# Optimization experiments

Measured on AMD Instinct MI355X. Metric: run time of the kernel, lower is better.

The kernel has to match this reference:

```python
import jax, jax.numpy as jnp
import numpy as np

B, S, D = 4, 1024, 1024
H = 16
HD = D // H  # 64
LN_EPS = 1e-5


def setup_inputs() -> dict:
    key = jax.random.key(0)
    ks = jax.random.split(key, 12)
    s = 1.0 / np.sqrt(D)
    return {
        "x": jax.random.normal(ks[0], (B, S, D), dtype=jnp.float32),
        "wq": jax.random.normal(ks[1], (D, D), dtype=jnp.float32) * s,
        "bq": jnp.zeros((D,), dtype=jnp.float32),
        "wk": jax.random.normal(ks[2], (D, D), dtype=jnp.float32) * s,
        "bk": jnp.zeros((D,), dtype=jnp.float32),
        "wv": jax.random.normal(ks[3], (D, D), dtype=jnp.float32) * s,
        "bv": jnp.zeros((D,), dtype=jnp.float32),
        "wl": jax.random.normal(ks[4], (D, D), dtype=jnp.float32) * s,
        "bl": jnp.zeros((D,), dtype=jnp.float32),
        "ln_g": jnp.ones((D,), dtype=jnp.float32),
        "ln_b": jnp.zeros((D,), dtype=jnp.float32),
    }


def _heads(t):
    # [B,S,D] -> [B,H,S,HD]
    return t.reshape(B, S, H, HD).transpose(0, 2, 1, 3)


def reference(x, wq, bq, wk, bk, wv, bv, wl, bl, ln_g, ln_b):
    q = _heads(x @ wq.T + bq)
    k = _heads(x @ wk.T + bk)
    v = _heads(x @ wv.T + bv)
    score = jnp.einsum("bhqd,bhkd->bhqk", q, k)
    # NOTE: unusual order — softmax first, THEN divide by sqrt(head_size)
    score = jax.nn.softmax(score, axis=-1) / jnp.sqrt(jnp.float32(HD))
    att = jnp.einsum("bhqk,bhkd->bhqd", score, v)
    att = att.transpose(0, 2, 1, 3).reshape(B, S, D)
    # residual added BEFORE the output linear
    y = (att + x) @ wl.T + bl
    # LayerNorm over last dim
    mu = jnp.mean(y, axis=-1, keepdims=True)
    var = jnp.mean(jnp.square(y - mu), axis=-1, keepdims=True)
    out = (y - mu) * jax.lax.rsqrt(var + LN_EPS) * ln_g + ln_b
    # dropout is identity in eval mode
    return out
```

## Files before the change

### kernel.cpp

```cpp
#include <hip/hip_runtime.h>
#include <cstdint>
#include <cstddef>

typedef __bf16 bf16;
typedef __bf16 bf16x4_t __attribute__((ext_vector_type(4)));
typedef __bf16 bf16x8_t __attribute__((ext_vector_type(8)));
typedef float f32x4_t __attribute__((ext_vector_type(4)));

#define DEV static __device__ __forceinline__

DEV void gload16(const void* g, void* l) {
  __builtin_amdgcn_global_load_lds((const __attribute__((address_space(1))) void*)g,
                                   (__attribute__((address_space(3))) void*)l, 16, 0, 0);
}

DEV f32x4_t mfma16(bf16x8_t a, bf16x8_t b, f32x4_t c) {
  return __builtin_amdgcn_mfma_f32_16x16x32_bf16(a, b, c, 0, 0, 0);
}

#define BAR __builtin_amdgcn_s_barrier()
#define FENCE asm volatile("" ::: "memory")
#define VMC(n) asm volatile("s_waitcnt vmcnt(" #n ")" ::: "memory")

__global__ __launch_bounds__(256) void k_convert(
    const float* __restrict__ x, const float* __restrict__ wq,
    const float* __restrict__ wk, const float* __restrict__ wv,
    const float* __restrict__ wl,
    bf16* __restrict__ xb, bf16* __restrict__ wqkvb, bf16* __restrict__ wlb) {
  const size_t M1 = (size_t)1 << 20;
  size_t i = ((size_t)blockIdx.x * 256 + threadIdx.x) * 4;
  const float* src; bf16* dst; size_t off;
  if (i < 4 * M1)      { src = x;  dst = xb;           off = i; }
  else if (i < 5 * M1) { src = wq; dst = wqkvb;        off = i - 4 * M1; }
  else if (i < 6 * M1) { src = wk; dst = wqkvb + M1;   off = i - 5 * M1; }
  else if (i < 7 * M1) { src = wv; dst = wqkvb + 2*M1; off = i - 6 * M1; }
  else                 { src = wl; dst = wlb;          off = i - 7 * M1; }
  f32x4_t v = *(const f32x4_t*)&src[off];
  bf16x4_t o;
  o[0] = (bf16)v[0]; o[1] = (bf16)v[1]; o[2] = (bf16)v[2]; o[3] = (bf16)v[3];
  *(bf16x4_t*)&dst[off] = o;
}

__global__ __launch_bounds__(256) void k_gemm_qkv(
    const bf16* __restrict__ W, const bf16* __restrict__ Xb,
    const float* __restrict__ bq, const float* __restrict__ bk,
    const float* __restrict__ bv,
    bf16* __restrict__ Q, bf16* __restrict__ Kc, bf16* __restrict__ VT) {
  __shared__ alignas(16) bf16 smem[16384];
  bf16* lA = smem;
  bf16* lB = smem + 8192;
  const int tid = threadIdx.x, wave = tid >> 6, lane = tid & 63;
  const int wm = (wave >> 1) * 64, wn = (wave & 1) * 64;
  const int fr = lane & 15, fg = lane >> 4;
  const int csw = (((lane & 7) ^ (lane >> 3)) << 3);
  const int m0 = blockIdx.x * 128, n0 = blockIdx.y * 128;

  f32x4_t acc[4][4];
  const f32x4_t vzero = {0.f, 0.f, 0.f, 0.f};
#pragma unroll
  for (int a = 0; a < 4; ++a)
#pragma unroll
    for (int c = 0; c < 4; ++c) acc[a][c] = vzero;

  const int rowoff = wave * 8 + (lane >> 3);

  for (int kt = 0; kt < 16; ++kt) {
#pragma unroll
    for (int i = 0; i < 4; ++i) {
      gload16(W + (size_t)(m0 + i * 32 + rowoff) * 1024 + kt * 64 + csw,
              &lA[(i * 32 + wave * 8) * 64]);
      gload16(Xb + (size_t)(n0 + i * 32 + rowoff) * 1024 + kt * 64 + csw,
              &lB[(i * 32 + wave * 8) * 64]);
    }
    __syncthreads();
    bf16x8_t af[4][2], bfr[4][2];
#pragma unroll
    for (int mi = 0; mi < 4; ++mi)
#pragma unroll
      for (int ks = 0; ks < 2; ++ks) {
        const int r = wm + mi * 16 + fr;
        af[mi][ks] = *(const bf16x8_t*)
            &lA[r * 64 + ((((ks << 2) + fg) ^ (fr & 7)) << 3)];
      }
#pragma unroll
    for (int ni = 0; ni < 4; ++ni)
#pragma unroll
      for (int ks = 0; ks < 2; ++ks) {
        const int r = wn + ni * 16 + fr;
        bfr[ni][ks] = *(const bf16x8_t*)
            &lB[r * 64 + ((((ks << 2) + fg) ^ (fr & 7)) << 3)];
      }
    __builtin_amdgcn_s_setprio(1);
#pragma unroll
    for (int ks = 0; ks < 2; ++ks)
#pragma unroll
      for (int mi = 0; mi < 4; ++mi)
#pragma unroll
        for (int ni = 0; ni < 4; ++ni)
          acc[mi][ni] = mfma16(af[mi][ks], bfr[ni][ks], acc[mi][ni]);
    __builtin_amdgcn_s_setprio(0);
    __syncthreads();
  }

  const int region = m0 >> 10;
  const float* bp = (region == 0) ? bq : ((region == 1) ? bk : bv);
  if (region < 2) {
    bf16* QK = (region == 0) ? Q : Kc;
#pragma unroll
    for (int mi = 0; mi < 4; ++mi) {
      const int f = (m0 & 1023) + wm + mi * 16 + fg * 4;
      const int h = f >> 6, d = f & 63;
#pragma unroll
      for (int ni = 0; ni < 4; ++ni) {
        const int t = n0 + wn + ni * 16 + fr;
        const int b = t >> 10, s = t & 1023;
        const int bh = b * 16 + h;
        f32x4_t v = acc[mi][ni];
        bf16x4_t o;
#pragma unroll
        for (int j = 0; j < 4; ++j) o[j] = (bf16)(v[j] + bp[f + j]);
        *(bf16x4_t*)&QK[((size_t)bh * 1024 + s) * 64 + d] = o;
      }
    }
  } else {
#pragma unroll
    for (int mi = 0; mi < 4; ++mi) {
      const int dl = wm + mi * 16 + fg * 4;
      const int floc = (m0 & 1023) + dl;
#pragma unroll
      for (int ni = 0; ni < 4; ++ni) {
        const int sl = wn + ni * 16 + fr;
        f32x4_t v = acc[mi][ni];
#pragma unroll
        for (int j = 0; j < 4; ++j) {
          const int d = dl + j;
          smem[d * 128 + (sl ^ ((d & 7) << 3))] = (bf16)(v[j] + bp[floc + j]);
        }
      }
    }
    __syncthreads();
    const int b = n0 >> 10;
#pragma unroll
    for (int i = 0; i < 8; ++i) {
      const int d = i * 16 + (tid >> 4);
      const int c = tid & 15;
      bf16x8_t vv = *(const bf16x8_t*)&smem[d * 128 + ((c ^ (d & 7)) << 3)];
      const int floc = (m0 & 1023) + d;
      const int h = floc >> 6, dd = floc & 63;
      const int sg = (n0 & 1023) + c * 8;
      *(bf16x8_t*)&VT[((size_t)(b * 16 + h) * 64 + dd) * 1024 + sg] = vv;
    }
  }
}

DEV void gemm_mainloop(const bf16* __restrict__ A, const bf16* __restrict__ B,
                       int m0, int n0,
                       bf16 (*lA)[128 * 64], bf16 (*lB)[128 * 64],
                       f32x4_t (&acc)[4][4]) {
  const int tid = threadIdx.x, wave = tid >> 6, lane = tid & 63;
  const int wm = (wave >> 1) * 64, wn = (wave & 1) * 64;
  const int fr = lane & 15, fg = lane >> 4;
  const int rowoff = wave * 8 + (lane >> 3);
  const int csw = (((lane & 7) ^ (lane >> 3)) << 3);

  auto STAGE = [&](int buf, int kt) {
#pragma unroll
    for (int i = 0; i < 4; ++i) {
      gload16(A + (size_t)(m0 + i * 32 + rowoff) * 1024 + kt * 64 + csw,
              &lA[buf][(i * 32 + wave * 8) * 64]);
      gload16(B + (size_t)(n0 + i * 32 + rowoff) * 1024 + kt * 64 + csw,
              &lB[buf][(i * 32 + wave * 8) * 64]);
    }
  };

  auto COMPUTE = [&](int buf) {
    bf16x8_t af[4][2], bfr[4][2];
#pragma unroll
    for (int mi = 0; mi < 4; ++mi)
#pragma unroll
      for (int ks = 0; ks < 2; ++ks) {
        const int r = wm + mi * 16 + fr;
        af[mi][ks] = *(const bf16x8_t*)
            &lA[buf][r * 64 + ((((ks << 2) + fg) ^ (fr & 7)) << 3)];
      }
#pragma unroll
    for (int ni = 0; ni < 4; ++ni)
#pragma unroll
      for (int ks = 0; ks < 2; ++ks) {
        const int r = wn + ni * 16 + fr;
        bfr[ni][ks] = *(const bf16x8_t*)
            &lB[buf][r * 64 + ((((ks << 2) + fg) ^ (fr & 7)) << 3)];
      }
    __builtin_amdgcn_s_setprio(1);
#pragma unroll
    for (int ks = 0; ks < 2; ++ks)
#pragma unroll
      for (int mi = 0; mi < 4; ++mi)
#pragma unroll
        for (int ni = 0; ni < 4; ++ni)
          acc[mi][ni] = mfma16(af[mi][ks], bfr[ni][ks], acc[mi][ni]);
    __builtin_amdgcn_s_setprio(0);
  };

  STAGE(0, 0);
  STAGE(1, 1);
  for (int t = 0; t < 15; ++t) {
    asm volatile("s_waitcnt vmcnt(8)" ::: "memory");
    __builtin_amdgcn_s_barrier();
    COMPUTE(t & 1);
    __builtin_amdgcn_s_barrier();
    if (t < 14) STAGE(t & 1, t + 2);
  }
  asm volatile("s_waitcnt vmcnt(0)" ::: "memory");
  __builtin_amdgcn_s_barrier();
  COMPUTE(1);
}

__global__ __launch_bounds__(256) void k_attn(
    const bf16* __restrict__ Q, const bf16* __restrict__ K,
    const bf16* __restrict__ VT, const float* __restrict__ X,
    bf16* __restrict__ ATTB) {
  __shared__ alignas(16) bf16 sm[16384];
  const int tid = threadIdx.x, wave = tid >> 6, lane = tid & 63;
  const int bh = blockIdx.x, qt = blockIdx.y;
  const int q0 = qt * 128 + wave * 32;
  const int fr = lane & 15, fg = lane >> 4;
  const int rx = (fr & 7) << 3;
  const f32x4_t vzero = {0.f, 0.f, 0.f, 0.f};

  bf16x8_t qf[2][2];
#pragma unroll
  for (int qi = 0; qi < 2; ++qi)
#pragma unroll
    for (int ks = 0; ks < 2; ++ks)
      qf[qi][ks] = *(const bf16x8_t*)
          &Q[((size_t)bh * 1024 + q0 + qi * 16 + fr) * 64 + ks * 32 + fg * 8];

  f32x4_t oacc[2][4];
  f32x4_t lsum4[2] = {vzero, vzero};
#pragma unroll
  for (int qi = 0; qi < 2; ++qi)
#pragma unroll
    for (int dj = 0; dj < 4; ++dj) oacc[qi][dj] = vzero;

  const int srow = lane >> 3;
  const int scolsw = (((lane & 7) ^ srow) * 8);

  auto STAGE = [&](int buf, int kv) {
    bf16* dK = sm + buf * 4096;
    bf16* dV = sm + 8192 + buf * 4096;
#pragma unroll
    for (int i = 0; i < 2; ++i) {
      const int c = wave * 2 + i;
      gload16(&K[((size_t)bh * 1024 + kv * 64 + c * 8 + srow) * 64 + scolsw],
              &dK[c * 512]);
      gload16(&VT[((size_t)bh * 64 + c * 8 + srow) * 1024 + kv * 64 + scolsw],
              &dV[c * 512]);
    }
  };

  auto TILE = [&](int cur) {
    const bf16* sK = sm + cur * 4096;
    const bf16* sV = sm + 8192 + cur * 4096;
    bf16x8_t kb[4][2];
#pragma unroll
    for (int kj = 0; kj < 4; ++kj)
#pragma unroll
      for (int ks = 0; ks < 2; ++ks) {
        const int r = kj * 16 + fr;
        kb[kj][ks] = *(const bf16x8_t*)&sK[r * 64 + ((ks * 32 + fg * 8) ^ rx)];
      }
    f32x4_t s[2][4];
#pragma unroll
    for (int qi = 0; qi < 2; ++qi)
#pragma unroll
      for (int kj = 0; kj < 4; ++kj) {
        f32x4_t z = vzero;
#pragma unroll
        for (int ks = 0; ks < 2; ++ks) z = mfma16(kb[kj][ks], qf[qi][ks], z);
        s[qi][kj] = z;
      }

    bf16x8_t vb[4][2];
#pragma unroll
    for (int dj = 0; dj < 4; ++dj)
#pragma unroll
      for (int ks = 0; ks < 2; ++ks) {
        const int r = dj * 16 + fr;
        const int c0 = ks * 32 + fg * 4;
        const int e0 = (c0 & 7) | ((((c0 >> 3) ^ (r & 7))) << 3);
        const int c1 = c0 + 16;
        const int e1 = (c1 & 7) | ((((c1 >> 3) ^ (r & 7))) << 3);
        bf16x4_t lo = *(const bf16x4_t*)&sV[r * 64 + e0];
        bf16x4_t hi = *(const bf16x4_t*)&sV[r * 64 + e1];
        bf16x8_t vv;
#pragma unroll
        for (int j = 0; j < 4; ++j) { vv[j] = lo[j]; vv[4 + j] = hi[j]; }
        vb[dj][ks] = vv;
      }

    bf16x8_t paf[2][2];
#pragma unroll
    for (int qi = 0; qi < 2; ++qi)
#pragma unroll
      for (int ks = 0; ks < 2; ++ks) {
        bf16x8_t pv;
#pragma unroll
        for (int h2 = 0; h2 < 2; ++h2)
#pragma unroll
          for (int j = 0; j < 4; ++j) {
            bf16 pb = (bf16)__expf(s[qi][2 * ks + h2][j]);
            lsum4[qi][j] += (float)pb;
            pv[h2 * 4 + j] = pb;
          }
        paf[qi][ks] = pv;
      }

#pragma unroll
    for (int qi = 0; qi < 2; ++qi)
#pragma unroll
      for (int dj = 0; dj < 4; ++dj)
#pragma unroll
        for (int ks = 0; ks < 2; ++ks)
          oacc[qi][dj] = mfma16(paf[qi][ks], vb[dj][ks], oacc[qi][dj]);
  };

  STAGE(0, 0);
  STAGE(1, 1);
  for (int kv = 0; kv < 15; ++kv) {
    VMC(4); BAR; FENCE;
    TILE(kv & 1);
    BAR; FENCE;
    if (kv < 14) STAGE(kv & 1, kv + 2);
  }
  VMC(0); BAR; FENCE;
  TILE(1);

  float lsum[2];
#pragma unroll
  for (int qi = 0; qi < 2; ++qi) {
    lsum[qi] = (lsum4[qi][0] + lsum4[qi][1]) + (lsum4[qi][2] + lsum4[qi][3]);
    lsum[qi] += __shfl_xor(lsum[qi], 16);
    lsum[qi] += __shfl_xor(lsum[qi], 32);
  }
  float rs[2][4];
#pragma unroll
  for (int qi = 0; qi < 2; ++qi)
#pragma unroll
    for (int j = 0; j < 4; ++j)
      rs[qi][j] = __shfl(lsum[qi], fg * 4 + j);

  BAR;
  bf16* lT = sm + wave * 2048;
#pragma unroll
  for (int qi = 0; qi < 2; ++qi)
#pragma unroll
    for (int dj = 0; dj < 4; ++dj)
#pragma unroll
      for (int j = 0; j < 4; ++j) {
        const int m = qi * 16 + fg * 4 + j;
        const int d = dj * 16 + fr;
        lT[m * 64 + (d ^ ((m & 7) << 3))] =
            (bf16)(oacc[qi][dj][j] / rs[qi][j] * 0.125f);
      }
  const int b = bh >> 4, h = bh & 15;
#pragma unroll
  for (int i = 0; i < 4; ++i) {
    const int row = i * 8 + (lane >> 3);
    const int col = (lane & 7) * 8;
    bf16x8_t av = *(const bf16x8_t*)&lT[row * 64 + (col ^ ((row & 7) << 3))];
    const size_t tok = (size_t)b * 1024 + q0 + row;
    const size_t fx = (size_t)h * 64 + col;
    f32x4_t x0 = *(const f32x4_t*)&X[tok * 1024 + fx];
    f32x4_t x1 = *(const f32x4_t*)&X[tok * 1024 + fx + 4];
    bf16x8_t o;
#pragma unroll
    for (int j = 0; j < 4; ++j) {
      o[j] = (bf16)((float)av[j] + x0[j]);
      o[4 + j] = (bf16)((float)av[4 + j] + x1[j]);
    }
    *(bf16x8_t*)&ATTB[tok * 1024 + fx] = o;
  }
}

__global__ __launch_bounds__(256, 2) void k_gemm_out(
    const bf16* __restrict__ Wl, const bf16* __restrict__ Ax,
    const float* __restrict__ bl, bf16* __restrict__ Y) {
  __shared__ alignas(16) bf16 lA[2][128 * 64];
  __shared__ alignas(16) bf16 lB[2][128 * 64];
  const f32x4_t vzero = {0.f, 0.f, 0.f, 0.f};
  f32x4_t acc[4][4];
#pragma unroll
  for (int a = 0; a < 4; ++a)
#pragma unroll
    for (int c = 0; c < 4; ++c) acc[a][c] = vzero;
  const int m0 = blockIdx.x * 128, n0 = blockIdx.y * 128;
  gemm_mainloop(Wl, Ax, m0, n0, lA, lB, acc);

  const int tid = threadIdx.x, wave = tid >> 6, lane = tid & 63;
  const int wm = (wave >> 1) * 64, wn = (wave & 1) * 64;
  const int fr = lane & 15, fg = lane >> 4;
#pragma unroll
  for (int mi = 0; mi < 4; ++mi) {
    const int f = m0 + wm + mi * 16 + fg * 4;
#pragma unroll
    for (int ni = 0; ni < 4; ++ni) {
      const int t = n0 + wn + ni * 16 + fr;
      f32x4_t v = acc[mi][ni];
      bf16x4_t o;
#pragma unroll
      for (int j = 0; j < 4; ++j) o[j] = (bf16)(v[j] + bl[f + j]);
      *(bf16x4_t*)&Y[(size_t)t * 1024 + f] = o;
    }
  }
}

__global__ __launch_bounds__(256) void k_ln(
    const bf16* __restrict__ Y, const float* __restrict__ g,
    const float* __restrict__ bta, float* __restrict__ OUT) {
  const int row = blockIdx.x, tid = threadIdx.x;
  const bf16* y = Y + (size_t)row * 1024;
  bf16x4_t yv = *(const bf16x4_t*)&y[tid * 4];
  f32x4_t v;
#pragma unroll
  for (int j = 0; j < 4; ++j) v[j] = (float)yv[j];
  float s = v[0] + v[1] + v[2] + v[3];
  float s2 = v[0]*v[0] + v[1]*v[1] + v[2]*v[2] + v[3]*v[3];
#pragma unroll
  for (int m = 1; m < 64; m <<= 1) {
    s += __shfl_xor(s, m);
    s2 += __shfl_xor(s2, m);
  }
  __shared__ float ps[4], ps2[4];
  const int wave = tid >> 6, lane = tid & 63;
  if (lane == 0) { ps[wave] = s; ps2[wave] = s2; }
  __syncthreads();
  s = ps[0] + ps[1] + ps[2] + ps[3];
  s2 = ps2[0] + ps2[1] + ps2[2] + ps2[3];
  const float mu = s * (1.f / 1024.f);
  const float var = s2 * (1.f / 1024.f) - mu * mu;
  const float rs = rsqrtf(var + 1e-5f);
  f32x4_t gg = *(const f32x4_t*)&g[tid * 4];
  f32x4_t bb = *(const f32x4_t*)&bta[tid * 4];
  f32x4_t o;
#pragma unroll
  for (int j = 0; j < 4; ++j) o[j] = (v[j] - mu) * rs * gg[j] + bb[j];
  *(f32x4_t*)&OUT[(size_t)row * 1024 + tid * 4] = o;
}

extern "C" void kernel_launch(void* const* d_in, const int* in_sizes, int n_in,
                              void* d_out, int out_size, void* d_ws, size_t ws_size,
                              hipStream_t stream) {
  (void)in_sizes; (void)n_in; (void)out_size; (void)ws_size;
  const float* x   = (const float*)d_in[0];
  const float* wq  = (const float*)d_in[1];
  const float* bq  = (const float*)d_in[2];
  const float* wk  = (const float*)d_in[3];
  const float* bk  = (const float*)d_in[4];
  const float* wv  = (const float*)d_in[5];
  const float* bv  = (const float*)d_in[6];
  const float* wl  = (const float*)d_in[7];
  const float* bl  = (const float*)d_in[8];
  const float* lng = (const float*)d_in[9];
  const float* lnb = (const float*)d_in[10];

  const size_t MB = (size_t)1 << 20;
  char* ws = (char*)d_ws;
  bf16* xb    = (bf16*)(ws);
  bf16* wqkvb = (bf16*)(ws + 8 * MB);
  bf16* wlb   = (bf16*)(ws + 14 * MB);
  bf16* Qb    = (bf16*)(ws + 16 * MB);
  bf16* Kb    = (bf16*)(ws + 24 * MB);
  bf16* VTb   = (bf16*)(ws + 32 * MB);
  bf16* attb  = (bf16*)(ws + 40 * MB);
  bf16* Y     = (bf16*)(ws + 16 * MB);

  k_convert<<<dim3(8192), dim3(256), 0, stream>>>(x, wq, wk, wv, wl, xb, wqkvb, wlb);
  k_gemm_qkv<<<dim3(24, 32), dim3(256), 0, stream>>>(wqkvb, xb, bq, bk, bv, Qb, Kb, VTb);
  k_attn<<<dim3(64, 8), dim3(256), 0, stream>>>(Qb, Kb, VTb, x, attb);
  k_gemm_out<<<dim3(8, 32), dim3(256), 0, stream>>>(wlb, attb, bl, Y);
  k_ln<<<dim3(4096), dim3(256), 0, stream>>>(Y, lng, lnb, (float*)d_out);
}
```

Before: 109.8 us.

## Shrink output GEMM tile to 64x128 and write attention epilogue directly

The output projection GEMM now uses 64x128 tiles instead of 128x128, doubling the grid from 256 to 512 blocks to better fill the GPU's compute units, at the cost of more redundant loads of the activation tile. The shared gemm_mainloop helper is inlined and specialized with adjusted staging and waitcnt. The attention epilogue drops its LDS transpose and barrier, writing scalar bf16 outputs with the residual added directly from registers. Those scalar global loads and stores are less coalesced than the previous 16-byte vector stores.

```diff
diff --git a/kernel.cpp b/kernel.cpp
--- a/kernel.cpp
+++ b/kernel.cpp
@@ -153,69 +153,6 @@
   }
 }
 
-DEV void gemm_mainloop(const bf16* __restrict__ A, const bf16* __restrict__ B,
-                       int m0, int n0,
-                       bf16 (*lA)[128 * 64], bf16 (*lB)[128 * 64],
-                       f32x4_t (&acc)[4][4]) {
-  const int tid = threadIdx.x, wave = tid >> 6, lane = tid & 63;
-  const int wm = (wave >> 1) * 64, wn = (wave & 1) * 64;
-  const int fr = lane & 15, fg = lane >> 4;
-  const int rowoff = wave * 8 + (lane >> 3);
-  const int csw = (((lane & 7) ^ (lane >> 3)) << 3);
-
-  auto STAGE = [&](int buf, int kt) {
-#pragma unroll
-    for (int i = 0; i < 4; ++i) {
-      gload16(A + (size_t)(m0 + i * 32 + rowoff) * 1024 + kt * 64 + csw,
-              &lA[buf][(i * 32 + wave * 8) * 64]);
-      gload16(B + (size_t)(n0 + i * 32 + rowoff) * 1024 + kt * 64 + csw,
-              &lB[buf][(i * 32 + wave * 8) * 64]);
-    }
-  };
-
-  auto COMPUTE = [&](int buf) {
-    bf16x8_t af[4][2], bfr[4][2];
-#pragma unroll
-    for (int mi = 0; mi < 4; ++mi)
-#pragma unroll
-      for (int ks = 0; ks < 2; ++ks) {
-        const int r = wm + mi * 16 + fr;
-        af[mi][ks] = *(const bf16x8_t*)
-            &lA[buf][r * 64 + ((((ks << 2) + fg) ^ (fr & 7)) << 3)];
-      }
-#pragma unroll
-    for (int ni = 0; ni < 4; ++ni)
-#pragma unroll
-      for (int ks = 0; ks < 2; ++ks) {
-        const int r = wn + ni * 16 + fr;
-        bfr[ni][ks] = *(const bf16x8_t*)
-            &lB[buf][r * 64 + ((((ks << 2) + fg) ^ (fr & 7)) << 3)];
-      }
-    __builtin_amdgcn_s_setprio(1);
-#pragma unroll
-    for (int ks = 0; ks < 2; ++ks)
-#pragma unroll
-      for (int mi = 0; mi < 4; ++mi)
-#pragma unroll
-        for (int ni = 0; ni < 4; ++ni)
-          acc[mi][ni] = mfma16(af[mi][ks], bfr[ni][ks], acc[mi][ni]);
-    __builtin_amdgcn_s_setprio(0);
-  };
-
-  STAGE(0, 0);
-  STAGE(1, 1);
-  for (int t = 0; t < 15; ++t) {
-    asm volatile("s_waitcnt vmcnt(8)" ::: "memory");
-    __builtin_amdgcn_s_barrier();
-    COMPUTE(t & 1);
-    __builtin_amdgcn_s_barrier();
-    if (t < 14) STAGE(t & 1, t + 2);
-  }
-  asm volatile("s_waitcnt vmcnt(0)" ::: "memory");
-  __builtin_amdgcn_s_barrier();
-  COMPUTE(1);
-}
-
 __global__ __launch_bounds__(256) void k_attn(
     const bf16* __restrict__ Q, const bf16* __restrict__ K,
     const bf16* __restrict__ VT, const float* __restrict__ X,
@@ -350,58 +287,96 @@
     for (int j = 0; j < 4; ++j)
       rs[qi][j] = __shfl(lsum[qi], fg * 4 + j);
 
-  BAR;
-  bf16* lT = sm + wave * 2048;
+  const int b = bh >> 4, h = bh & 15;
 #pragma unroll
   for (int qi = 0; qi < 2; ++qi)
 #pragma unroll
     for (int dj = 0; dj < 4; ++dj)
 #pragma unroll
       for (int j = 0; j < 4; ++j) {
-        const int m = qi * 16 + fg * 4 + j;
-        const int d = dj * 16 + fr;
-        lT[m * 64 + (d ^ ((m & 7) << 3))] =
-            (bf16)(oacc[qi][dj][j] / rs[qi][j] * 0.125f);
-      }
-  const int b = bh >> 4, h = bh & 15;
-#pragma unroll
-  for (int i = 0; i < 4; ++i) {
-    const int row = i * 8 + (lane >> 3);
-    const int col = (lane & 7) * 8;
-    bf16x8_t av = *(const bf16x8_t*)&lT[row * 64 + (col ^ ((row & 7) << 3))];
-    const size_t tok = (size_t)b * 1024 + q0 + row;
-    const size_t fx = (size_t)h * 64 + col;
-    f32x4_t x0 = *(const f32x4_t*)&X[tok * 1024 + fx];
-    f32x4_t x1 = *(const f32x4_t*)&X[tok * 1024 + fx + 4];
-    bf16x8_t o;
-#pragma unroll
-    for (int j = 0; j < 4; ++j) {
-      o[j] = (bf16)((float)av[j] + x0[j]);
-      o[4 + j] = (bf16)((float)av[4 + j] + x1[j]);
-    }
-    *(bf16x8_t*)&ATTB[tok * 1024 + fx] = o;
-  }
+        const int s_ = q0 + qi * 16 + fg * 4 + j;
+        const int d_ = dj * 16 + fr;
+        const size_t tok = (size_t)b * 1024 + s_;
+        const size_t fidx = (size_t)h * 64 + d_;
+        float val = oacc[qi][dj][j] / rs[qi][j] * 0.125f + X[tok * 1024 + fidx];
+        ATTB[tok * 1024 + fidx] = (bf16)val;
+      }
 }
 
 __global__ __launch_bounds__(256, 2) void k_gemm_out(
     const bf16* __restrict__ Wl, const bf16* __restrict__ Ax,
     const float* __restrict__ bl, bf16* __restrict__ Y) {
-  __shared__ alignas(16) bf16 lA[2][128 * 64];
+  __shared__ alignas(16) bf16 lA[2][64 * 64];
   __shared__ alignas(16) bf16 lB[2][128 * 64];
+  const int tid = threadIdx.x, wave = tid >> 6, lane = tid & 63;
+  const int wm = (wave >> 1) * 32, wn = (wave & 1) * 64;
+  const int fr = lane & 15, fg = lane >> 4;
+  const int srow = lane >> 3;
+  const int csw = (((lane & 7) ^ srow) << 3);
+  const int m0 = blockIdx.x * 64, n0 = blockIdx.y * 128;
+
+  f32x4_t acc[2][4];
   const f32x4_t vzero = {0.f, 0.f, 0.f, 0.f};
-  f32x4_t acc[4][4];
-#pragma unroll
-  for (int a = 0; a < 4; ++a)
+#pragma unroll
+  for (int a = 0; a < 2; ++a)
 #pragma unroll
     for (int c = 0; c < 4; ++c) acc[a][c] = vzero;
-  const int m0 = blockIdx.x * 128, n0 = blockIdx.y * 128;
-  gemm_mainloop(Wl, Ax, m0, n0, lA, lB, acc);
-
-  const int tid = threadIdx.x, wave = tid >> 6, lane = tid & 63;
-  const int wm = (wave >> 1) * 64, wn = (wave & 1) * 64;
-  const int fr = lane & 15, fg = lane >> 4;
-#pragma unroll
-  for (int mi = 0; mi < 4; ++mi) {
+
+  auto STAGE = [&](int buf, int kt) {
+#pragma unroll
+    for (int i = 0; i < 2; ++i)
+      gload16(Wl + (size_t)(m0 + wave * 16 + i * 8 + srow) * 1024 + kt * 64 + csw,
+              &lA[buf][(wave * 16 + i * 8) * 64]);
+#pragma unroll
+    for (int i = 0; i < 4; ++i)
+      gload16(Ax + (size_t)(n0 + wave * 32 + i * 8 + srow) * 1024 + kt * 64 + csw,
+              &lB[buf][(wave * 32 + i * 8) * 64]);
+  };
+
+  auto COMPUTE = [&](int buf) {
+    bf16x8_t af[2][2], bfr[4][2];
+#pragma unroll
+    for (int mi = 0; mi < 2; ++mi)
+#pragma unroll
+      for (int ks = 0; ks < 2; ++ks) {
+        const int r = wm + mi * 16 + fr;
+        af[mi][ks] = *(const bf16x8_t*)
+            &lA[buf][r * 64 + ((((ks << 2) + fg) ^ (fr & 7)) << 3)];
+      }
+#pragma unroll
+    for (int ni = 0; ni < 4; ++ni)
+#pragma unroll
+      for (int ks = 0; ks < 2; ++ks) {
+        const int r = wn + ni * 16 + fr;
+        bfr[ni][ks] = *(const bf16x8_t*)
+            &lB[buf][r * 64 + ((((ks << 2) + fg) ^ (fr & 7)) << 3)];
+      }
+    __builtin_amdgcn_s_setprio(1);
+#pragma unroll
+    for (int ks = 0; ks < 2; ++ks)
+#pragma unroll
+      for (int mi = 0; mi < 2; ++mi)
+#pragma unroll
+        for (int ni = 0; ni < 4; ++ni)
+          acc[mi][ni] = mfma16(af[mi][ks], bfr[ni][ks], acc[mi][ni]);
+    __builtin_amdgcn_s_setprio(0);
+  };
+
+  STAGE(0, 0);
+  STAGE(1, 1);
+  for (int t = 0; t < 15; ++t) {
+    asm volatile("s_waitcnt vmcnt(6)" ::: "memory");
+    __builtin_amdgcn_s_barrier();
+    COMPUTE(t & 1);
+    __builtin_amdgcn_s_barrier();
+    if (t < 14) STAGE(t & 1, t + 2);
+  }
+  asm volatile("s_waitcnt vmcnt(0)" ::: "memory");
+  __builtin_amdgcn_s_barrier();
+  COMPUTE(1);
+
+#pragma unroll
+  for (int mi = 0; mi < 2; ++mi) {
     const int f = m0 + wm + mi * 16 + fg * 4;
 #pragma unroll
     for (int ni = 0; ni < 4; ++ni) {
@@ -478,6 +453,6 @@
   k_convert<<<dim3(8192), dim3(256), 0, stream>>>(x, wq, wk, wv, wl, xb, wqkvb, wlb);
   k_gemm_qkv<<<dim3(24, 32), dim3(256), 0, stream>>>(wqkvb, xb, bq, bk, bv, Qb, Kb, VTb);
   k_attn<<<dim3(64, 8), dim3(256), 0, stream>>>(Qb, Kb, VTb, x, attb);
-  k_gemm_out<<<dim3(8, 32), dim3(256), 0, stream>>>(wlb, attb, bl, Y);
+  k_gemm_out<<<dim3(16, 32), dim3(256), 0, stream>>>(wlb, attb, bl, Y);
   k_ln<<<dim3(4096), dim3(256), 0, stream>>>(Y, lng, lnb, (float*)d_out);
 }
```

New measurement: 104.7 us, median of 2. 1.05x faster.
